# Kernel optimization log

Hardware: AMD Instinct MI355X
Metric: run time of the kernel (lower is better)

Reference implementation:

```python
import jax, jax.numpy as jnp
import numpy as np

D_MODEL = 1024
NUM_HEADS = 16
D_K = D_MODEL // NUM_HEADS


def setup_inputs() -> dict:
    key = jax.random.key(0)
    ks = jax.random.split(key, 8)
    B, S = 2, 2048
    std = 1.0 / np.sqrt(D_MODEL)
    return {
        "Q": jax.random.normal(ks[0], (B, S, D_MODEL), jnp.float32),
        "K": jax.random.normal(ks[1], (B, S, D_MODEL), jnp.float32),
        "V": jax.random.normal(ks[2], (B, S, D_MODEL), jnp.float32),
        "W_q": jax.random.normal(ks[3], (D_MODEL, D_MODEL), jnp.float32) * std,
        "W_k": jax.random.normal(ks[4], (D_MODEL, D_MODEL), jnp.float32) * std,
        "W_v": jax.random.normal(ks[5], (D_MODEL, D_MODEL), jnp.float32) * std,
        "W_o": jax.random.normal(ks[6], (D_MODEL, D_MODEL), jnp.float32) * std,
        "b_o": jnp.zeros((D_MODEL,), jnp.float32),
    }


def reference(Q, K, V, W_q, W_k, W_v, W_o, b_o):
    B, S, _ = Q.shape
    H, dk = NUM_HEADS, D_K
    scale = 1.0 / np.sqrt(dk)
    # project and split heads: [B, H, S, dk]
    def split_heads(x, W):
        return (x @ W.T).reshape(B, -1, H, dk).transpose(0, 2, 1, 3)
    q = split_heads(Q, W_q)
    k = split_heads(K, W_k)
    v = split_heads(V, W_v)
    # scores: [B, H, S, S]
    scores = jnp.einsum("bhqd,bhkd->bhqk", q, k) * scale
    causal_mask = jnp.triu(jnp.ones((S, S), bool), k=1)
    scores = jnp.where(causal_mask, -jnp.inf, scores)
    attn = jax.nn.softmax(scores, axis=-1)
    out = jnp.einsum("bhqk,bhkd->bhqd", attn, v)  # [B, H, S, dk]
    out = out.transpose(0, 2, 1, 3).reshape(B, S, H * dk)
    out = out @ W_o.T + b_o
    return out, attn
```

## Files before the change

kernel.cpp:

```cpp
#include <hip/hip_runtime.h>
#include <hip/hip_bf16.h>

#define SEQ 2048
#define BATCH 2
#define NH 16
#define DK 64
#define DM 1024

typedef __bf16 bf16;
typedef __bf16 bf16x8 __attribute__((ext_vector_type(8)));
typedef float f32x4 __attribute__((ext_vector_type(4)));
typedef short s16x4 __attribute__((ext_vector_type(4)));

#define MFMA16(a,b,c) __builtin_amdgcn_mfma_f32_16x16x32_bf16(a,b,c,0,0,0)
#define NEG_BIG (-1.0e30f)

#define GLL16(gsrc, ldst) __builtin_amdgcn_global_load_lds( \
    (const __attribute__((address_space(1))) void*)(gsrc), \
    (__attribute__((address_space(3))) void*)(ldst), 16, 0, 0)

__device__ __forceinline__ bf16x8 ld8(const bf16* p){ return *(const bf16x8*)p; }

__device__ __forceinline__ bf16x8 frag_bf16lds(const bf16* Ls, int row, int lq){
    int c = lq ^ (row&3);
    return *(const bf16x8*)((const char*)Ls + row*64 + c*16);
}

__device__ __forceinline__ bf16x8 frag_f32lds(const float* Ls, int row, int lq){
    int c0 = ((lq<<1)    ) ^ (row&7);
    int c1 = ((lq<<1) | 1) ^ (row&7);
    const float* p = Ls + row*32;
    f32x4 a = *(const f32x4*)(p + c0*4);
    f32x4 b = *(const f32x4*)(p + c1*4);
    bf16x8 r;
    #pragma unroll
    for (int i=0;i<4;i++){ r[i] = (bf16)a[i]; r[i+4] = (bf16)b[i]; }
    return r;
}

__global__ __launch_bounds__(256) void cvt_kernel(
    const float* __restrict__ Q,  const float* __restrict__ K,  const float* __restrict__ V,
    const float* __restrict__ Wq, const float* __restrict__ Wk, const float* __restrict__ Wv,
    bf16* __restrict__ Qb, bf16* __restrict__ Kb, bf16* __restrict__ Vb,
    bf16* __restrict__ Wqb, bf16* __restrict__ Wkb, bf16* __restrict__ Wvb)
{
    const int a = blockIdx.y;
    const float* src = (a==0)?Q:(a==1)?K:(a==2)?V:(a==3)?Wq:(a==4)?Wk:Wv;
    bf16* dst        = (a==0)?Qb:(a==1)?Kb:(a==2)?Vb:(a==3)?Wqb:(a==4)?Wkb:Wvb;
    const int n4 = (a<3) ? (BATCH*SEQ*DM)/4 : (DM*DM)/4;
    for (int i = blockIdx.x*256 + threadIdx.x; i < n4; i += gridDim.x*256){
        f32x4 v = ((const f32x4*)src)[i];
        bf16 o[4];
        #pragma unroll
        for (int j=0;j<4;j++) o[j] = (bf16)v[j];
        ((s16x4*)dst)[i] = *(const s16x4*)o;
    }
}

__global__ __launch_bounds__(256) void qkv_proj_kernel(
    const bf16* __restrict__ Qb, const bf16* __restrict__ Kb, const bf16* __restrict__ Vb,
    const bf16* __restrict__ Wqb, const bf16* __restrict__ Wkb, const bf16* __restrict__ Wvb,
    bf16* __restrict__ q_s, bf16* __restrict__ k_s, bf16* __restrict__ vt_s)
{
    __shared__ __align__(16) bf16 As[128*32];
    __shared__ __align__(16) bf16 Bs[128*32];
    const int z = blockIdx.z;
    const bf16* X = (z==0) ? Qb  : (z==1) ? Kb  : Vb;
    const bf16* W = (z==0) ? Wqb : (z==1) ? Wkb : Wvb;
    bf16* out     = (z==0) ? q_s : (z==1) ? k_s : vt_s;

    const int tid  = threadIdx.x;
    const int lane = tid & 63;
    const int w    = tid >> 6;
    const int lr = lane & 15, lq = lane >> 4;
    const int mt  = (w>>1)*64;
    const int nt0 = (w&1)*64;
    const int m0 = blockIdx.y*128;
    const int n0 = blockIdx.x*128;

    f32x4 acc[4][4] = {};
    for (int k0 = 0; k0 < DM; k0 += 32) {
        if (k0) __syncthreads();
        #pragma unroll
        for (int i=0;i<2;i++){
            int ci  = i*256 + tid;
            int row = ci >> 2, ch = ci & 3;
            int gc  = (ch ^ (row&3)) << 3;
            GLL16(X + (size_t)(m0+row)*DM + k0 + gc, (char*)As + ci*16);
            GLL16(W + (size_t)(n0+row)*DM + k0 + gc, (char*)Bs + ci*16);
        }
        __syncthreads();
        bf16x8 af[4], bfr[4];
        #pragma unroll
        for (int mi=0;mi<4;mi++) af[mi]  = frag_bf16lds(As, mt  + mi*16 + lr, lq);
        #pragma unroll
        for (int ni=0;ni<4;ni++) bfr[ni] = frag_bf16lds(Bs, nt0 + ni*16 + lr, lq);
        #pragma unroll
        for (int mi=0;mi<4;mi++)
            #pragma unroll
            for (int ni=0;ni<4;ni++)
                acc[mi][ni] = MFMA16(af[mi], bfr[ni], acc[mi][ni]);
    }

    if (z == 2) {
        #pragma unroll
        for (int mi=0;mi<4;mi++)
        #pragma unroll
        for (int ni=0;ni<4;ni++){
            int row = m0 + mt + mi*16 + lq*4;
            int col = n0 + nt0 + ni*16 + lr;
            int b = row >> 11, s = row & (SEQ-1);
            int h = col >> 6,  dd = col & 63;
            bf16 pk[4];
            #pragma unroll
            for (int r=0;r<4;r++) pk[r] = (bf16)acc[mi][ni][r];
            *(s16x4*)&out[((size_t)((b*NH + h)*DK + dd))*SEQ + s] = *(const s16x4*)pk;
        }
    } else {
        #pragma unroll
        for (int mi=0;mi<4;mi++)
        #pragma unroll
        for (int ni=0;ni<4;ni++)
        #pragma unroll
        for (int r=0;r<4;r++) {
            int row = m0 + mt + mi*16 + lq*4 + r;
            int col = n0 + nt0 + ni*16 + lr;
            int b = row >> 11, s = row & (SEQ-1);
            int h = col >> 6,  dd = col & 63;
            out[((size_t)(b*NH + h))*SEQ*DK + (size_t)s*DK + dd] = (bf16)acc[mi][ni][r];
        }
    }
}

__device__ __forceinline__ void load_ktile(const bf16* __restrict__ kp,
                                           int kt, int lr, int lq, bf16x8* kf){
    #pragma unroll
    for (int ks=0;ks<2;ks++)
        #pragma unroll
        for (int nt=0;nt<4;nt++)
            kf[ks*4+nt] = ld8(kp + (size_t)(kt*64 + nt*16 + lr)*DK + ks*32 + lq*8);
}

__device__ __forceinline__ void mfma_scores(const bf16x8* qf, const bf16x8* kf, f32x4* s){
    const f32x4 z4 = {0.f,0.f,0.f,0.f};
    #pragma unroll
    for (int nt=0;nt<4;nt++) s[nt] = z4;
    #pragma unroll
    for (int ks=0;ks<2;ks++)
        #pragma unroll
        for (int nt=0;nt<4;nt++)
            s[nt] = MFMA16(qf[ks], kf[ks*4+nt], s[nt]);
}

__global__ __launch_bounds__(128,4) void attn_kernel(
    const bf16* __restrict__ q_s, const bf16* __restrict__ k_s,
    const bf16* __restrict__ vt_s,
    float* __restrict__ attn_out, bf16* __restrict__ ao)
{
    __shared__ __align__(16) bf16 P[2][16][72];
    const int bh = blockIdx.x;
    const int lane = threadIdx.x & 63, w = threadIdx.x >> 6;
    const int lr = lane & 15, lq = lane >> 4;
    const int qtile = w ? (127 - (int)blockIdx.y) : (int)blockIdx.y;
    const int qw0   = qtile*16;
    const int ktmax = qw0 >> 6;

    const bf16* qp = q_s  + (size_t)bh*SEQ*DK;
    const bf16* kp = k_s  + (size_t)bh*SEQ*DK;
    const bf16* vp = vt_s + (size_t)bh*DK*SEQ;
    float* ab = attn_out + (size_t)bh*SEQ*SEQ;

    bf16x8 qf[2];
    qf[0] = ld8(qp + (size_t)(qw0+lr)*DK + lq*8);
    qf[1] = ld8(qp + (size_t)(qw0+lr)*DK + 32 + lq*8);

    float lsum[4] = {0.f,0.f,0.f,0.f};
    bf16x8 kf[8];
    load_ktile(kp, 0, lr, lq, kf);
    for (int kt=0; kt<ktmax; kt++) {
        bf16x8 kn[8];
        load_ktile(kp, kt+1, lr, lq, kn);
        f32x4 s[4];
        mfma_scores(qf, kf, s);
        #pragma unroll
        for (int nt=0;nt<4;nt++)
            #pragma unroll
            for (int r=0;r<4;r++)
                lsum[r] += __expf(s[nt][r]*0.125f);
        #pragma unroll
        for (int i=0;i<8;i++) kf[i] = kn[i];
    }
    {
        f32x4 s[4];
        mfma_scores(qf, kf, s);
        #pragma unroll
        for (int nt=0;nt<4;nt++)
            #pragma unroll
            for (int r=0;r<4;r++){
                float v = s[nt][r]*0.125f;
                if ((ktmax*64 + nt*16 + lr) > (qw0 + lq*4 + r)) v = NEG_BIG;
                lsum[r] += __expf(v);
            }
    }
    float inv_l[4];
    #pragma unroll
    for (int r=0;r<4;r++){
        float t = lsum[r];
        t += __shfl_xor(t,1); t += __shfl_xor(t,2);
        t += __shfl_xor(t,4); t += __shfl_xor(t,8);
        inv_l[r] = 1.0f / t;
    }

    f32x4 o[4] = {};
    for (int kt=0; kt<=ktmax; kt++) {
        load_ktile(kp, kt, lr, lq, kf);
        f32x4 s[4];
        mfma_scores(qf, kf, s);
        bf16x8 vf[8];
        #pragma unroll
        for (int ks=0;ks<2;ks++)
            #pragma unroll
            for (int nt=0;nt<4;nt++)
                vf[ks*4+nt] = ld8(vp + (size_t)(nt*16+lr)*SEQ + kt*64 + ks*32 + lq*8);
        if (kt < ktmax) {
            #pragma unroll
            for (int nt=0;nt<4;nt++)
                #pragma unroll
                for (int r=0;r<4;r++){
                    float p = __expf(s[nt][r]*0.125f) * inv_l[r];
                    ab[(size_t)(qw0 + lq*4 + r)*SEQ + kt*64 + nt*16 + lr] = p;
                    P[w][lq*4+r][nt*16+lr] = (bf16)p;
                }
        } else {
            #pragma unroll
            for (int nt=0;nt<4;nt++)
                #pragma unroll
                for (int r=0;r<4;r++){
                    float v = s[nt][r]*0.125f;
                    if ((kt*64 + nt*16 + lr) > (qw0 + lq*4 + r)) v = NEG_BIG;
                    float p = __expf(v) * inv_l[r];
                    ab[(size_t)(qw0 + lq*4 + r)*SEQ + kt*64 + nt*16 + lr] = p;
                    P[w][lq*4+r][nt*16+lr] = (bf16)p;
                }
        }
        __asm__ __volatile__("" ::: "memory");
        #pragma unroll
        for (int ks=0;ks<2;ks++){
            bf16x8 pf = *(const bf16x8*)(&P[w][lr][ks*32 + lq*8]);
            #pragma unroll
            for (int nt=0;nt<4;nt++)
                o[nt] = MFMA16(pf, vf[ks*4+nt], o[nt]);
        }
    }

    const int b = bh >> 4, h = bh & 15;
    #pragma unroll
    for (int nt=0;nt<4;nt++)
        #pragma unroll
        for (int r=0;r<4;r++){
            int qrow = qw0 + lq*4 + r;
            ao[(size_t)(b*SEQ + qrow)*DM + h*64 + nt*16 + lr] = (bf16)o[nt][r];
        }

    int cstart = (ktmax+1)*64;
    if (cstart < SEQ) {
        const f32x4 z4 = {0.f,0.f,0.f,0.f};
        float* rp = ab + (size_t)(qw0 + (lane>>2))*SEQ;
        for (int c4 = (cstart>>2) + (lane&3); c4 < (SEQ>>2); c4 += 4)
            *(f32x4*)(rp + c4*4) = z4;
    }
}

__global__ __launch_bounds__(256) void out_proj_kernel(
    const bf16* __restrict__ Xa, const float* __restrict__ Wo,
    const float* __restrict__ bo, float* __restrict__ out)
{
    __shared__ __align__(16) bf16  Asb[128*32];
    __shared__ __align__(16) float Bs [128*32];
    const int tid  = threadIdx.x;
    const int lane = tid & 63;
    const int w    = tid >> 6;
    const int lr = lane & 15, lq = lane >> 4;
    const int mt  = (w>>1)*64;
    const int nt0 = (w&1)*64;
    const int m0 = blockIdx.y*128;
    const int n0 = blockIdx.x*128;

    f32x4 acc[4][4] = {};
    for (int k0 = 0; k0 < DM; k0 += 32) {
        if (k0) __syncthreads();
        #pragma unroll
        for (int i=0;i<2;i++){
            int ci  = i*256 + tid;
            int row = ci >> 2, ch = ci & 3;
            GLL16(Xa + (size_t)(m0+row)*DM + k0 + ((ch ^ (row&3))<<3),
                  (char*)Asb + ci*16);
        }
        #pragma unroll
        for (int i=0;i<4;i++){
            int ci  = i*256 + tid;
            int row = ci >> 3, ch = ci & 7;
            GLL16(Wo + (size_t)(n0+row)*DM + k0 + ((ch ^ (row&7))<<2),
                  (char*)Bs + ci*16);
        }
        __syncthreads();
        bf16x8 af[4], bfr[4];
        #pragma unroll
        for (int mi=0;mi<4;mi++) af[mi]  = frag_bf16lds(Asb, mt  + mi*16 + lr, lq);
        #pragma unroll
        for (int ni=0;ni<4;ni++) bfr[ni] = frag_f32lds (Bs,  nt0 + ni*16 + lr, lq);
        #pragma unroll
        for (int mi=0;mi<4;mi++)
            #pragma unroll
            for (int ni=0;ni<4;ni++)
                acc[mi][ni] = MFMA16(af[mi], bfr[ni], acc[mi][ni]);
    }
    #pragma unroll
    for (int mi=0;mi<4;mi++)
    #pragma unroll
    for (int ni=0;ni<4;ni++)
    #pragma unroll
    for (int r=0;r<4;r++) {
        int row = m0 + mt + mi*16 + lq*4 + r;
        int col = n0 + nt0 + ni*16 + lr;
        out[(size_t)row*DM + col] = acc[mi][ni][r] + bo[col];
    }
}

extern "C" void kernel_launch(void* const* d_in, const int* in_sizes, int n_in,
                              void* d_out, int out_size, void* d_ws, size_t ws_size,
                              hipStream_t stream)
{
    const float* Q  = (const float*)d_in[0];
    const float* K  = (const float*)d_in[1];
    const float* V  = (const float*)d_in[2];
    const float* Wq = (const float*)d_in[3];
    const float* Wk = (const float*)d_in[4];
    const float* Wv = (const float*)d_in[5];
    const float* Wo = (const float*)d_in[6];
    const float* bo = (const float*)d_in[7];
    float* out = (float*)d_out;

    bf16* ws = (bf16*)d_ws;
    const size_t NTOK = (size_t)BATCH*SEQ*DM;
    bf16* q_s  = ws;
    bf16* k_s  = ws + NTOK;
    bf16* vt_s = ws + 2*NTOK;
    bf16* ao   = ws + 3*NTOK;

    float* ab  = out + NTOK;
    bf16* Qb   = (bf16*)ab;
    bf16* Kb   = Qb + NTOK;
    bf16* Vb   = Qb + 2*NTOK;
    bf16* Wqb  = Qb + 3*NTOK;
    bf16* Wkb  = Wqb + (size_t)DM*DM;
    bf16* Wvb  = Wqb + 2*(size_t)DM*DM;

    cvt_kernel<<<dim3(256,6), 256, 0, stream>>>(Q,K,V,Wq,Wk,Wv, Qb,Kb,Vb,Wqb,Wkb,Wvb);
    qkv_proj_kernel<<<dim3(8,32,3), 256, 0, stream>>>(Qb,Kb,Vb,Wqb,Wkb,Wvb, q_s,k_s,vt_s);
    attn_kernel<<<dim3(32,64), 128, 0, stream>>>(q_s,k_s,vt_s, ab, ao);
    out_proj_kernel<<<dim3(8,32), 256, 0, stream>>>(ao,Wo,bo,out);
}
```

Measured before the change: 815.5 us.

## Process two query subtiles per wave in attention and pre-convert W_o to bf16

The attention kernel now has each wave handle 32 query rows (two 16-row subtiles), so every K and V tile load is reused across twice as many rows. The grid is halved, occupancy hints drop from 4 to 2, and the P staging buffer gains an XOR swizzle to avoid LDS bank conflicts. Separately, W_o is converted to bf16 by a new kernel into the freed q_s workspace, so the output projection uses the shared bf16 GEMM tile instead of converting fp32 weights on every LDS fragment read. The costs are higher register pressure with fewer waves to hide latency, and coarser causal load balance.

```diff
diff --git a/kernel.cpp b/kernel.cpp
--- a/kernel.cpp
+++ b/kernel.cpp
@@ -24,18 +24,6 @@
 __device__ __forceinline__ bf16x8 frag_bf16lds(const bf16* Ls, int row, int lq){
     int c = lq ^ (row&3);
     return *(const bf16x8*)((const char*)Ls + row*64 + c*16);
-}
-
-__device__ __forceinline__ bf16x8 frag_f32lds(const float* Ls, int row, int lq){
-    int c0 = ((lq<<1)    ) ^ (row&7);
-    int c1 = ((lq<<1) | 1) ^ (row&7);
-    const float* p = Ls + row*32;
-    f32x4 a = *(const f32x4*)(p + c0*4);
-    f32x4 b = *(const f32x4*)(p + c1*4);
-    bf16x8 r;
-    #pragma unroll
-    for (int i=0;i<4;i++){ r[i] = (bf16)a[i]; r[i+4] = (bf16)b[i]; }
-    return r;
 }
 
 __global__ __launch_bounds__(256) void cvt_kernel(
@@ -54,6 +42,48 @@
         #pragma unroll
         for (int j=0;j<4;j++) o[j] = (bf16)v[j];
         ((s16x4*)dst)[i] = *(const s16x4*)o;
+    }
+}
+
+__global__ __launch_bounds__(256) void cvtW_kernel(
+    const float* __restrict__ W, bf16* __restrict__ Wb)
+{
+    const int n4 = (DM*DM)/4;
+    for (int i = blockIdx.x*256 + threadIdx.x; i < n4; i += gridDim.x*256){
+        f32x4 v = ((const f32x4*)W)[i];
+        bf16 o[4];
+        #pragma unroll
+        for (int j=0;j<4;j++) o[j] = (bf16)v[j];
+        ((s16x4*)Wb)[i] = *(const s16x4*)o;
+    }
+}
+
+__device__ __forceinline__ void gemm_tile_bf16(
+    const bf16* __restrict__ X, const bf16* __restrict__ W,
+    bf16* As, bf16* Bs, int m0, int n0, int tid, int mt, int nt0,
+    int lr, int lq, f32x4 acc[4][4])
+{
+    for (int k0 = 0; k0 < DM; k0 += 32) {
+        if (k0) __syncthreads();
+        #pragma unroll
+        for (int i=0;i<2;i++){
+            int ci  = i*256 + tid;
+            int row = ci >> 2, ch = ci & 3;
+            int gc  = (ch ^ (row&3)) << 3;
+            GLL16(X + (size_t)(m0+row)*DM + k0 + gc, (char*)As + ci*16);
+            GLL16(W + (size_t)(n0+row)*DM + k0 + gc, (char*)Bs + ci*16);
+        }
+        __syncthreads();
+        bf16x8 af[4], bfr[4];
+        #pragma unroll
+        for (int mi=0;mi<4;mi++) af[mi]  = frag_bf16lds(As, mt  + mi*16 + lr, lq);
+        #pragma unroll
+        for (int ni=0;ni<4;ni++) bfr[ni] = frag_bf16lds(Bs, nt0 + ni*16 + lr, lq);
+        #pragma unroll
+        for (int mi=0;mi<4;mi++)
+            #pragma unroll
+            for (int ni=0;ni<4;ni++)
+                acc[mi][ni] = MFMA16(af[mi], bfr[ni], acc[mi][ni]);
     }
 }
 
@@ -79,28 +109,7 @@
     const int n0 = blockIdx.x*128;
 
     f32x4 acc[4][4] = {};
-    for (int k0 = 0; k0 < DM; k0 += 32) {
-        if (k0) __syncthreads();
-        #pragma unroll
-        for (int i=0;i<2;i++){
-            int ci  = i*256 + tid;
-            int row = ci >> 2, ch = ci & 3;
-            int gc  = (ch ^ (row&3)) << 3;
-            GLL16(X + (size_t)(m0+row)*DM + k0 + gc, (char*)As + ci*16);
-            GLL16(W + (size_t)(n0+row)*DM + k0 + gc, (char*)Bs + ci*16);
-        }
-        __syncthreads();
-        bf16x8 af[4], bfr[4];
-        #pragma unroll
-        for (int mi=0;mi<4;mi++) af[mi]  = frag_bf16lds(As, mt  + mi*16 + lr, lq);
-        #pragma unroll
-        for (int ni=0;ni<4;ni++) bfr[ni] = frag_bf16lds(Bs, nt0 + ni*16 + lr, lq);
-        #pragma unroll
-        for (int mi=0;mi<4;mi++)
-            #pragma unroll
-            for (int ni=0;ni<4;ni++)
-                acc[mi][ni] = MFMA16(af[mi], bfr[ni], acc[mi][ni]);
-    }
+    gemm_tile_bf16(X, W, As, Bs, m0, n0, tid, mt, nt0, lr, lq, acc);
 
     if (z == 2) {
         #pragma unroll
@@ -152,131 +161,154 @@
             s[nt] = MFMA16(qf[ks], kf[ks*4+nt], s[nt]);
 }
 
-__global__ __launch_bounds__(128,4) void attn_kernel(
+__global__ __launch_bounds__(128,2) void attn_kernel(
     const bf16* __restrict__ q_s, const bf16* __restrict__ k_s,
     const bf16* __restrict__ vt_s,
     float* __restrict__ attn_out, bf16* __restrict__ ao)
 {
-    __shared__ __align__(16) bf16 P[2][16][72];
+    __shared__ __align__(16) bf16 P[2][32][64];
     const int bh = blockIdx.x;
     const int lane = threadIdx.x & 63, w = threadIdx.x >> 6;
     const int lr = lane & 15, lq = lane >> 4;
-    const int qtile = w ? (127 - (int)blockIdx.y) : (int)blockIdx.y;
-    const int qw0   = qtile*16;
-    const int ktmax = qw0 >> 6;
+    const int qtile = w ? (63 - (int)blockIdx.y) : (int)blockIdx.y;
+    const int qw0   = qtile*32;
+    const int ktmax = (qw0 + 31) >> 6;
 
     const bf16* qp = q_s  + (size_t)bh*SEQ*DK;
     const bf16* kp = k_s  + (size_t)bh*SEQ*DK;
     const bf16* vp = vt_s + (size_t)bh*DK*SEQ;
     float* ab = attn_out + (size_t)bh*SEQ*SEQ;
-
-    bf16x8 qf[2];
-    qf[0] = ld8(qp + (size_t)(qw0+lr)*DK + lq*8);
-    qf[1] = ld8(qp + (size_t)(qw0+lr)*DK + 32 + lq*8);
-
-    float lsum[4] = {0.f,0.f,0.f,0.f};
+    char* Pw = (char*)&P[w][0][0];
+
+    bf16x8 qf[2][2];
+    #pragma unroll
+    for (int qi=0;qi<2;qi++)
+        #pragma unroll
+        for (int ks=0;ks<2;ks++)
+            qf[qi][ks] = ld8(qp + (size_t)(qw0+qi*16+lr)*DK + ks*32 + lq*8);
+
+    float lsum[2][4] = {};
     bf16x8 kf[8];
     load_ktile(kp, 0, lr, lq, kf);
     for (int kt=0; kt<ktmax; kt++) {
         bf16x8 kn[8];
         load_ktile(kp, kt+1, lr, lq, kn);
-        f32x4 s[4];
-        mfma_scores(qf, kf, s);
-        #pragma unroll
-        for (int nt=0;nt<4;nt++)
-            #pragma unroll
-            for (int r=0;r<4;r++)
-                lsum[r] += __expf(s[nt][r]*0.125f);
+        #pragma unroll
+        for (int qi=0;qi<2;qi++){
+            f32x4 s[4];
+            mfma_scores(qf[qi], kf, s);
+            #pragma unroll
+            for (int nt=0;nt<4;nt++)
+                #pragma unroll
+                for (int r=0;r<4;r++)
+                    lsum[qi][r] += __expf(s[nt][r]*0.125f);
+        }
         #pragma unroll
         for (int i=0;i<8;i++) kf[i] = kn[i];
     }
     {
-        f32x4 s[4];
-        mfma_scores(qf, kf, s);
-        #pragma unroll
-        for (int nt=0;nt<4;nt++)
-            #pragma unroll
-            for (int r=0;r<4;r++){
-                float v = s[nt][r]*0.125f;
-                if ((ktmax*64 + nt*16 + lr) > (qw0 + lq*4 + r)) v = NEG_BIG;
-                lsum[r] += __expf(v);
-            }
-    }
-    float inv_l[4];
-    #pragma unroll
-    for (int r=0;r<4;r++){
-        float t = lsum[r];
-        t += __shfl_xor(t,1); t += __shfl_xor(t,2);
-        t += __shfl_xor(t,4); t += __shfl_xor(t,8);
-        inv_l[r] = 1.0f / t;
-    }
-
-    f32x4 o[4] = {};
+        #pragma unroll
+        for (int qi=0;qi<2;qi++){
+            f32x4 s[4];
+            mfma_scores(qf[qi], kf, s);
+            #pragma unroll
+            for (int nt=0;nt<4;nt++)
+                #pragma unroll
+                for (int r=0;r<4;r++){
+                    float v = s[nt][r]*0.125f;
+                    if ((ktmax*64 + nt*16 + lr) > (qw0 + qi*16 + lq*4 + r)) v = NEG_BIG;
+                    lsum[qi][r] += __expf(v);
+                }
+        }
+    }
+    float inv_l[2][4];
+    #pragma unroll
+    for (int qi=0;qi<2;qi++)
+        #pragma unroll
+        for (int r=0;r<4;r++){
+            float t = lsum[qi][r];
+            t += __shfl_xor(t,1); t += __shfl_xor(t,2);
+            t += __shfl_xor(t,4); t += __shfl_xor(t,8);
+            inv_l[qi][r] = 1.0f / t;
+        }
+
+    f32x4 o[2][4] = {};
     for (int kt=0; kt<=ktmax; kt++) {
         load_ktile(kp, kt, lr, lq, kf);
-        f32x4 s[4];
-        mfma_scores(qf, kf, s);
         bf16x8 vf[8];
         #pragma unroll
         for (int ks=0;ks<2;ks++)
             #pragma unroll
             for (int nt=0;nt<4;nt++)
                 vf[ks*4+nt] = ld8(vp + (size_t)(nt*16+lr)*SEQ + kt*64 + ks*32 + lq*8);
-        if (kt < ktmax) {
-            #pragma unroll
-            for (int nt=0;nt<4;nt++)
-                #pragma unroll
-                for (int r=0;r<4;r++){
-                    float p = __expf(s[nt][r]*0.125f) * inv_l[r];
-                    ab[(size_t)(qw0 + lq*4 + r)*SEQ + kt*64 + nt*16 + lr] = p;
-                    P[w][lq*4+r][nt*16+lr] = (bf16)p;
-                }
-        } else {
-            #pragma unroll
-            for (int nt=0;nt<4;nt++)
-                #pragma unroll
-                for (int r=0;r<4;r++){
-                    float v = s[nt][r]*0.125f;
-                    if ((kt*64 + nt*16 + lr) > (qw0 + lq*4 + r)) v = NEG_BIG;
-                    float p = __expf(v) * inv_l[r];
-                    ab[(size_t)(qw0 + lq*4 + r)*SEQ + kt*64 + nt*16 + lr] = p;
-                    P[w][lq*4+r][nt*16+lr] = (bf16)p;
-                }
+        #pragma unroll
+        for (int qi=0;qi<2;qi++){
+            f32x4 s[4];
+            mfma_scores(qf[qi], kf, s);
+            if (kt < ktmax) {
+                #pragma unroll
+                for (int nt=0;nt<4;nt++)
+                    #pragma unroll
+                    for (int r=0;r<4;r++){
+                        float p = __expf(s[nt][r]*0.125f) * inv_l[qi][r];
+                        int row = qi*16 + lq*4 + r, col = nt*16 + lr;
+                        ab[(size_t)(qw0 + row)*SEQ + kt*64 + col] = p;
+                        *(bf16*)(Pw + row*128 + ((col*2) ^ ((row&7)<<4))) = (bf16)p;
+                    }
+            } else {
+                #pragma unroll
+                for (int nt=0;nt<4;nt++)
+                    #pragma unroll
+                    for (int r=0;r<4;r++){
+                        float v = s[nt][r]*0.125f;
+                        if ((kt*64 + nt*16 + lr) > (qw0 + qi*16 + lq*4 + r)) v = NEG_BIG;
+                        float p = __expf(v) * inv_l[qi][r];
+                        int row = qi*16 + lq*4 + r, col = nt*16 + lr;
+                        ab[(size_t)(qw0 + row)*SEQ + kt*64 + col] = p;
+                        *(bf16*)(Pw + row*128 + ((col*2) ^ ((row&7)<<4))) = (bf16)p;
+                    }
+            }
         }
         __asm__ __volatile__("" ::: "memory");
         #pragma unroll
-        for (int ks=0;ks<2;ks++){
-            bf16x8 pf = *(const bf16x8*)(&P[w][lr][ks*32 + lq*8]);
-            #pragma unroll
-            for (int nt=0;nt<4;nt++)
-                o[nt] = MFMA16(pf, vf[ks*4+nt], o[nt]);
-        }
+        for (int qi=0;qi<2;qi++)
+            #pragma unroll
+            for (int ks=0;ks<2;ks++){
+                int row = qi*16 + lr;
+                bf16x8 pf = *(const bf16x8*)(Pw + row*128
+                                + ((ks*64 + lq*16) ^ ((row&7)<<4)));
+                #pragma unroll
+                for (int nt=0;nt<4;nt++)
+                    o[qi][nt] = MFMA16(pf, vf[ks*4+nt], o[qi][nt]);
+            }
     }
 
     const int b = bh >> 4, h = bh & 15;
     #pragma unroll
-    for (int nt=0;nt<4;nt++)
-        #pragma unroll
-        for (int r=0;r<4;r++){
-            int qrow = qw0 + lq*4 + r;
-            ao[(size_t)(b*SEQ + qrow)*DM + h*64 + nt*16 + lr] = (bf16)o[nt][r];
-        }
+    for (int qi=0;qi<2;qi++)
+        #pragma unroll
+        for (int nt=0;nt<4;nt++)
+            #pragma unroll
+            for (int r=0;r<4;r++){
+                int qrow = qw0 + qi*16 + lq*4 + r;
+                ao[(size_t)(b*SEQ + qrow)*DM + h*64 + nt*16 + lr] = (bf16)o[qi][nt][r];
+            }
 
     int cstart = (ktmax+1)*64;
     if (cstart < SEQ) {
         const f32x4 z4 = {0.f,0.f,0.f,0.f};
-        float* rp = ab + (size_t)(qw0 + (lane>>2))*SEQ;
-        for (int c4 = (cstart>>2) + (lane&3); c4 < (SEQ>>2); c4 += 4)
+        float* rp = ab + (size_t)(qw0 + (lane>>1))*SEQ;
+        for (int c4 = (cstart>>2) + (lane&1); c4 < (SEQ>>2); c4 += 2)
             *(f32x4*)(rp + c4*4) = z4;
     }
 }
 
 __global__ __launch_bounds__(256) void out_proj_kernel(
-    const bf16* __restrict__ Xa, const float* __restrict__ Wo,
+    const bf16* __restrict__ Xa, const bf16* __restrict__ Wob,
     const float* __restrict__ bo, float* __restrict__ out)
 {
-    __shared__ __align__(16) bf16  Asb[128*32];
-    __shared__ __align__(16) float Bs [128*32];
+    __shared__ __align__(16) bf16 As[128*32];
+    __shared__ __align__(16) bf16 Bs[128*32];
     const int tid  = threadIdx.x;
     const int lane = tid & 63;
     const int w    = tid >> 6;
@@ -287,34 +319,8 @@
     const int n0 = blockIdx.x*128;
 
     f32x4 acc[4][4] = {};
-    for (int k0 = 0; k0 < DM; k0 += 32) {
-        if (k0) __syncthreads();
-        #pragma unroll
-        for (int i=0;i<2;i++){
-            int ci  = i*256 + tid;
-            int row = ci >> 2, ch = ci & 3;
-            GLL16(Xa + (size_t)(m0+row)*DM + k0 + ((ch ^ (row&3))<<3),
-                  (char*)Asb + ci*16);
-        }
-        #pragma unroll
-        for (int i=0;i<4;i++){
-            int ci  = i*256 + tid;
-            int row = ci >> 3, ch = ci & 7;
-            GLL16(Wo + (size_t)(n0+row)*DM + k0 + ((ch ^ (row&7))<<2),
-                  (char*)Bs + ci*16);
-        }
-        __syncthreads();
-        bf16x8 af[4], bfr[4];
-        #pragma unroll
-        for (int mi=0;mi<4;mi++) af[mi]  = frag_bf16lds(Asb, mt  + mi*16 + lr, lq);
-        #pragma unroll
-        for (int ni=0;ni<4;ni++) bfr[ni] = frag_f32lds (Bs,  nt0 + ni*16 + lr, lq);
-        #pragma unroll
-        for (int mi=0;mi<4;mi++)
-            #pragma unroll
-            for (int ni=0;ni<4;ni++)
-                acc[mi][ni] = MFMA16(af[mi], bfr[ni], acc[mi][ni]);
-    }
+    gemm_tile_bf16(Xa, Wob, As, Bs, m0, n0, tid, mt, nt0, lr, lq, acc);
+
     #pragma unroll
     for (int mi=0;mi<4;mi++)
     #pragma unroll
@@ -356,8 +362,11 @@
     bf16* Wkb  = Wqb + (size_t)DM*DM;
     bf16* Wvb  = Wqb + 2*(size_t)DM*DM;
 
+    bf16* Wob  = q_s;
+
     cvt_kernel<<<dim3(256,6), 256, 0, stream>>>(Q,K,V,Wq,Wk,Wv, Qb,Kb,Vb,Wqb,Wkb,Wvb);
     qkv_proj_kernel<<<dim3(8,32,3), 256, 0, stream>>>(Qb,Kb,Vb,Wqb,Wkb,Wvb, q_s,k_s,vt_s);
-    attn_kernel<<<dim3(32,64), 128, 0, stream>>>(q_s,k_s,vt_s, ab, ao);
-    out_proj_kernel<<<dim3(8,32), 256, 0, stream>>>(ao,Wo,bo,out);
-}
+    attn_kernel<<<dim3(32,32), 128, 0, stream>>>(q_s,k_s,vt_s, ab, ao);
+    cvtW_kernel<<<dim3(128), 256, 0, stream>>>(Wo, Wob);
+    out_proj_kernel<<<dim3(8,32), 256, 0, stream>>>(ao,Wob,bo,out);
+}
```

Result: faster. 763.1 us (-6.4%).
